# Performance work log

Hardware: AMD Instinct MI355X
Metric: run time of the kernel (lower is better)

Reference implementation:

```python
import jax, jax.numpy as jnp
import numpy as np

N_NODES = 100000
N_EDGES = 1000000
D = 64
HID = 64
OUT = 64
N_CLS = 10
N_GRAPHS = 512
BN_EPS = 1e-5


def setup_inputs() -> dict:
    key = jax.random.key(0)
    ks = jax.random.split(key, 16)
    inp = {
        "x": jax.random.normal(ks[0], (N_NODES, D), dtype=jnp.float32),
        "edge_index": jax.random.randint(ks[1], (2, N_EDGES), 0, N_NODES, dtype=jnp.int32),
        "batch": jnp.sort(jax.random.randint(ks[2], (N_NODES,), 0, N_GRAPHS, dtype=jnp.int32)),
    }
    def lin(k, fi, fo):
        lim = 1.0 / np.sqrt(fi)
        kw, kb = jax.random.split(k)
        return (jax.random.uniform(kw, (fi, fo), minval=-lim, maxval=lim, dtype=jnp.float32),
                jax.random.uniform(kb, (fo,), minval=-lim, maxval=lim, dtype=jnp.float32))
    # conv0 MLP([64,64,64]) with BN after first linear
    inp["w0a"], inp["b0a"] = lin(ks[3], D, HID)
    inp["g0"] = jnp.ones((HID,), jnp.float32); inp["be0"] = jnp.zeros((HID,), jnp.float32)
    inp["m0"] = jnp.zeros((HID,), jnp.float32); inp["v0"] = jnp.ones((HID,), jnp.float32)
    inp["w0b"], inp["b0b"] = lin(ks[4], HID, HID)
    # conv1 MLP([64,64,64])
    inp["w1a"], inp["b1a"] = lin(ks[5], HID, HID)
    inp["g1"] = jnp.ones((HID,), jnp.float32); inp["be1"] = jnp.zeros((HID,), jnp.float32)
    inp["m1"] = jnp.zeros((HID,), jnp.float32); inp["v1"] = jnp.ones((HID,), jnp.float32)
    inp["w1b"], inp["b1b"] = lin(ks[6], HID, OUT)
    # classifier
    inp["wc"], inp["bc"] = lin(ks[7], OUT, N_CLS)
    return inp


def _bn_eval(h, g, b, m, v):
    return (h - m) * jax.lax.rsqrt(v + BN_EPS) * g + b


def _mlp(h, wa, ba, g, be, m, v, wb, bb):
    # Linear -> BN -> ReLU -> (dropout eval=identity) -> Linear
    h = h @ wa + ba
    h = jax.nn.relu(_bn_eval(h, g, be, m, v))
    return h @ wb + bb


def _gin_conv(h, src, dst, wa, ba, g, be, m, v, wb, bb):
    # GINConv eps=0: mlp(x + sum_{j->i} x_j), messages scatter-added at dst
    agg = jax.ops.segment_sum(h[src], dst, num_segments=N_NODES)
    return _mlp(h + agg, wa, ba, g, be, m, v, wb, bb)


def reference(x, edge_index, batch,
              w0a, b0a, g0, be0, m0, v0, w0b, b0b,
              w1a, b1a, g1, be1, m1, v1, w1b, b1b,
              wc, bc):
    src, dst = edge_index[0], edge_index[1]
    h = _gin_conv(x, src, dst, w0a, b0a, g0, be0, m0, v0, w0b, b0b)
    h = jax.nn.relu(h)  # dropout is identity in eval
    h = _gin_conv(h, src, dst, w1a, b1a, g1, be1, m1, v1, w1b, b1b)
    # global mean pool over batch indices
    sums = jax.ops.segment_sum(h, batch, num_segments=N_GRAPHS)
    cnts = jax.ops.segment_sum(jnp.ones((h.shape[0],), h.dtype), batch, num_segments=N_GRAPHS)
    pooled = sums / jnp.maximum(cnts, 1.0)[:, None]
    return pooled @ wc + bc
```

## Files before the change

### kernel.cpp

```cpp
#include <hip/hip_runtime.h>

#define N_NODES 100000
#define N_EDGES 1000000
#define N_GRAPHS 512
#define N_CLS 10
#define BN_EPS 1e-5f

#define SCAN_NB 200
#define NTILES2 3125

typedef _Float16 half8 __attribute__((ext_vector_type(8)));
typedef _Float16 half4v __attribute__((ext_vector_type(4)));
typedef float floatx4 __attribute__((ext_vector_type(4)));

__global__ __launch_bounds__(256) void prep_kernel(
    const float* __restrict__ x, _Float16* __restrict__ xh,
    const int* __restrict__ batch, const int* __restrict__ dstI,
    int* __restrict__ deg, int* __restrict__ rank,
    const float* __restrict__ w0a, const float* __restrict__ b0a,
    const float* __restrict__ g0, const float* __restrict__ be0,
    const float* __restrict__ m0, const float* __restrict__ v0,
    const float* __restrict__ w0b,
    const float* __restrict__ w1a, const float* __restrict__ b1a,
    const float* __restrict__ g1, const float* __restrict__ be1,
    const float* __restrict__ m1, const float* __restrict__ v1,
    const float* __restrict__ w1b,
    int* __restrict__ gstart,
    _Float16* __restrict__ wHi, _Float16* __restrict__ wLo,
    float* __restrict__ b1p0, float* __restrict__ b1p1) {
    const int gid = blockIdx.x * 256 + threadIdx.x;

    if (gid < 1600000) {
        float4 v = ((const float4*)x)[gid];
        half4v h = {(_Float16)v.x, (_Float16)v.y, (_Float16)v.z, (_Float16)v.w};
        ((half4v*)xh)[gid] = h;
    }

    if (gid < N_EDGES)
        rank[gid] = atomicAdd(&deg[dstI[gid]], 1);

    if (gid <= N_NODES) {
        int bcur = (gid < N_NODES) ? batch[gid] : N_GRAPHS;
        int bprev = (gid > 0) ? batch[gid - 1] : -1;
        for (int g = bprev + 1; g <= bcur; ++g) gstart[g] = gid;
    }

    if (gid < 16384) {
        const int e = gid & 4095, mat = gid >> 12;
        const int jj = e & 7, lane = (e >> 3) & 63, c = (e >> 9) & 3, k0 = (e >> 11) & 1;
        const int k = k0 * 32 + (lane >> 4) * 8 + jj;
        const int col = c * 16 + (lane & 15);
        float val;
        if (mat == 0)      val = w0a[k * 64 + col] * (rsqrtf(v0[col] + BN_EPS) * g0[col]);
        else if (mat == 1) val = w0b[k * 64 + col];
        else if (mat == 2) val = w1a[k * 64 + col] * (rsqrtf(v1[col] + BN_EPS) * g1[col]);
        else               val = w1b[k * 64 + col];
        _Float16 hi = (_Float16)val;
        wHi[gid] = hi;
        wLo[gid] = (_Float16)(val - (float)hi);
    }

    if (gid >= 16384 && gid < 16512) {
        int t = gid - 16384;
        if (t < 64) {
            float s = rsqrtf(v0[t] + BN_EPS) * g0[t];
            b1p0[t] = (b0a[t] - m0[t]) * s + be0[t];
        } else {
            t -= 64;
            float s = rsqrtf(v1[t] + BN_EPS) * g1[t];
            b1p1[t] = (b1a[t] - m1[t]) * s + be1[t];
        }
    }
}

__global__ __launch_bounds__(256) void scanA_kernel(const int* __restrict__ deg,
                                                    int* __restrict__ bsum) {
    __shared__ int sh[256];
    const int base = blockIdx.x * 512;
    const int t = threadIdx.x;
    int a = 0, b = 0;
    if (base + t < N_NODES) a = deg[base + t];
    if (base + 256 + t < N_NODES) b = deg[base + 256 + t];
    sh[t] = a + b;
    __syncthreads();
#pragma unroll
    for (int off = 128; off > 0; off >>= 1) {
        if (t < off) sh[t] += sh[t + off];
        __syncthreads();
    }
    if (t == 0) bsum[blockIdx.x] = sh[0];
}

__global__ __launch_bounds__(256) void scanC_kernel(const int* __restrict__ deg,
                                                    const int* __restrict__ bsum,
                                                    int* __restrict__ rowptr) {
    __shared__ int sh[256];
    __shared__ int sboff[256];
    const int base = blockIdx.x * 512;
    const int t = threadIdx.x;

    const int bv = (t < SCAN_NB) ? bsum[t] : 0;
    sboff[t] = bv;

    const int i0 = base + 2 * t, i1 = i0 + 1;
    const int d0 = (i0 < N_NODES) ? deg[i0] : 0;
    const int d1 = (i1 < N_NODES) ? deg[i1] : 0;
    const int p = d0 + d1;
    sh[t] = p;
    __syncthreads();
#pragma unroll
    for (int off = 1; off < 256; off <<= 1) {
        int u = (t >= off) ? sh[t - off] : 0;
        int ub = (t >= off) ? sboff[t - off] : 0;
        __syncthreads();
        sh[t] += u;
        sboff[t] += ub;
        __syncthreads();
    }
    const int myoff = (blockIdx.x == 0) ? 0 : sboff[blockIdx.x - 1];
    const int excl = myoff + sh[t] - p;
    if (i0 < N_NODES) rowptr[i0] = excl;
    if (i1 < N_NODES) rowptr[i1] = excl + d0;
    if (blockIdx.x == 0 && t == 0) rowptr[N_NODES] = N_EDGES;
}

__global__ __launch_bounds__(256) void fill_kernel(const int* __restrict__ srcI,
                                                   const int* __restrict__ dstI,
                                                   const int* __restrict__ rank,
                                                   const int* __restrict__ rowptr,
                                                   int* __restrict__ sortedSrc) {
    int e = blockIdx.x * 256 + threadIdx.x;
    if (e >= N_EDGES) return;
    sortedSrc[rowptr[dstI[e]] + rank[e]] = srcI[e];
}

__device__ __forceinline__ int swz(int row, int col) {
    return row * 64 + (col ^ ((row & 7) << 3));
}

__device__ __forceinline__ void idx_stage(const int* __restrict__ srcList, int rpv,
                                          int mq, int nodeSel, int slotSel, int& idxOwn) {
    const int rr0 = __shfl(rpv, mq * 4 + nodeSel, 64);
    const int rr1 = __shfl(rpv, mq * 4 + nodeSel + 1, 64);
    const int c = rr1 - rr0;
    const int e0 = (c > 0) ? min(slotSel, c - 1) : 0;
    int pos = rr0 + e0;
    pos = min(pos, N_EDGES - 1);
    idxOwn = srcList[pos];
}

__device__ __forceinline__ void rows_stage(const _Float16* __restrict__ in, int rpv,
                                           int mq, int strip0, int eoff, int lf,
                                           int idxOwn, half4v (&vT)[4][4], half4v (&sS)[4]) {
    const int m0 = mq * 4;
#pragma unroll
    for (int i = 0; i < 4; ++i) {
        sS[i] = (half4v){0, 0, 0, 0};
        if (eoff == 0)
            sS[i] = *(const half4v*)(in + (size_t)(strip0 + m0 + i) * 64 + lf * 4);
    }
#pragma unroll
    for (int i = 0; i < 4; ++i) {
        const int rr0 = __builtin_amdgcn_readlane(rpv, m0 + i);
        const int rr1 = __builtin_amdgcn_readlane(rpv, m0 + i + 1);
        const int cI = rr1 - rr0;
        const int g = (min(cI, 16) + 3) >> 2;
#pragma unroll
        for (int k = 0; k < 4; ++k) {
            vT[i][k] = (half4v){0, 0, 0, 0};
            if (k < g) {
                const int id = __shfl(idxOwn, i * 16 + 4 * k + eoff, 64);
                vT[i][k] = *(const half4v*)(in + (size_t)id * 64 + lf * 4);
            }
        }
    }
}

__device__ __forceinline__ void consume_stage(const _Float16* __restrict__ in,
                                              const int* __restrict__ srcList, int rpv,
                                              int mq, int eoff, int lf, int j,
                                              const half4v (&vT)[4][4], const half4v (&sS)[4],
                                              _Float16* aggH, _Float16* aggL) {
    const int m0 = mq * 4;
#pragma unroll
    for (int i = 0; i < 4; ++i) {
        const int rr0 = __builtin_amdgcn_readlane(rpv, m0 + i);
        const int rr1 = __builtin_amdgcn_readlane(rpv, m0 + i + 1);
        const int cI = rr1 - rr0;
        float aR[4] = {0.f, 0.f, 0.f, 0.f};
#pragma unroll
        for (int k = 0; k < 4; ++k) {
            if (4 * k + eoff < cI) {
                aR[0] += (float)vT[i][k].x; aR[1] += (float)vT[i][k].y;
                aR[2] += (float)vT[i][k].z; aR[3] += (float)vT[i][k].w;
            }
        }
        for (int eb = 16; eb < cI; eb += 16) {
#pragma unroll
            for (int k = 0; k < 4; ++k) {
                const int e_ = eb + 4 * k + eoff;
                if (e_ < cI) {
                    const int id = srcList[rr0 + e_];
                    half4v t = *(const half4v*)(in + (size_t)id * 64 + lf * 4);
                    aR[0] += (float)t.x; aR[1] += (float)t.y;
                    aR[2] += (float)t.z; aR[3] += (float)t.w;
                }
            }
        }
        if (eoff == 0) {
            aR[0] += (float)sS[i].x; aR[1] += (float)sS[i].y;
            aR[2] += (float)sS[i].z; aR[3] += (float)sS[i].w;
        }
#pragma unroll
        for (int q = 0; q < 4; ++q) {
            aR[q] += __shfl_xor(aR[q], 16, 64);
            aR[q] += __shfl_xor(aR[q], 32, 64);
        }
        if (j < 16) {
            half4v hi, lo;
#pragma unroll
            for (int q = 0; q < 4; ++q) {
                hi[q] = (_Float16)aR[q];
                lo[q] = (_Float16)(aR[q] - (float)hi[q]);
            }
            const int idx = swz(m0 + i, 4 * j);
            *(half4v*)(aggH + idx) = hi;
            *(half4v*)(aggL + idx) = lo;
        }
    }
}

#define SBAR() __builtin_amdgcn_sched_barrier(0)

template <int POOL>
__global__ __launch_bounds__(128, 2) void conv_mfma(
    const _Float16* __restrict__ in, const int* __restrict__ rowptr,
    const int* __restrict__ srcList,
    const _Float16* __restrict__ wH1, const _Float16* __restrict__ wL1,
    const _Float16* __restrict__ wH2, const _Float16* __restrict__ wL2,
    const float* __restrict__ b1, const float* __restrict__ b2,
    _Float16* __restrict__ out, const int* __restrict__ batch,
    float* __restrict__ pooled) {
    __shared__ __align__(16) unsigned char scratch[2][4096];

    const int tid = threadIdx.x;
    const int j = tid & 63, wv = tid >> 6;
    const int eoff = j >> 4;
    const int lf = j & 15;
    const int base = blockIdx.x * 32;
    const int strip0 = base + wv * 16;

    int bb = 0;
    if (POOL) bb = batch[strip0 + min(j, 15)];

    const int rpv = rowptr[strip0 + min(j, 16)];

    _Float16* aggH = (_Float16*)scratch[wv];
    _Float16* aggL = aggH + 1024;

    {
        int idxA, idxB, idxC;
        half4v vA[4][4], vB[4][4], sA[4], sB[4];

        idx_stage(srcList, rpv, 0, eoff, lf, idxA);
        idx_stage(srcList, rpv, 1, eoff, lf, idxB);
        SBAR();
        rows_stage(in, rpv, 0, strip0, eoff, lf, idxA, vA, sA);
        SBAR();
        idx_stage(srcList, rpv, 2, eoff, lf, idxC);
        SBAR();
        rows_stage(in, rpv, 1, strip0, eoff, lf, idxB, vB, sB);
        SBAR();
        consume_stage(in, srcList, rpv, 0, eoff, lf, j, vA, sA, aggH, aggL);
        SBAR();
        idx_stage(srcList, rpv, 3, eoff, lf, idxA);
        SBAR();
        rows_stage(in, rpv, 2, strip0, eoff, lf, idxC, vA, sA);
        SBAR();
        consume_stage(in, srcList, rpv, 1, eoff, lf, j, vB, sB, aggH, aggL);
        SBAR();
        rows_stage(in, rpv, 3, strip0, eoff, lf, idxA, vB, sB);
        SBAR();
        consume_stage(in, srcList, rpv, 2, eoff, lf, j, vA, sA, aggH, aggL);
        SBAR();
        consume_stage(in, srcList, rpv, 3, eoff, lf, j, vB, sB, aggH, aggL);
    }

    const int l15 = j & 15, quad = j >> 4;
    const floatx4 vzero = {0.f, 0.f, 0.f, 0.f};

    floatx4 acc[4] = {vzero, vzero, vzero, vzero};
    {
#pragma unroll
        for (int k0 = 0; k0 < 2; ++k0) {
            const int aidx = swz(l15, quad * 8 + k0 * 32);
            half8 aH = *(const half8*)(aggH + aidx);
            half8 aL = *(const half8*)(aggL + aidx);
#pragma unroll
            for (int c = 0; c < 4; ++c) {
                const int fo = ((k0 * 4 + c) * 64 + j) * 8;
                half8 bH = *(const half8*)(wH1 + fo);
                half8 bL = *(const half8*)(wL1 + fo);
                acc[c] = __builtin_amdgcn_mfma_f32_16x16x32_f16(aH, bH, acc[c], 0, 0, 0);
                acc[c] = __builtin_amdgcn_mfma_f32_16x16x32_f16(aL, bH, acc[c], 0, 0, 0);
                acc[c] = __builtin_amdgcn_mfma_f32_16x16x32_f16(aH, bL, acc[c], 0, 0, 0);
            }
        }
    }
    _Float16* hH = aggH;
    _Float16* hL = aggL;
#pragma unroll
    for (int c = 0; c < 4; ++c) {
        const float bv = b1[c * 16 + l15];
#pragma unroll
        for (int r = 0; r < 4; ++r) {
            const int idx = swz(quad * 4 + r, c * 16 + l15);
            float v = acc[c][r] + bv;
            v = fmaxf(v, 0.f);
            const _Float16 hi = (_Float16)v;
            hH[idx] = hi;
            hL[idx] = (_Float16)(v - (float)hi);
        }
    }

    floatx4 acc2[4] = {vzero, vzero, vzero, vzero};
    {
#pragma unroll
        for (int k0 = 0; k0 < 2; ++k0) {
            const int aidx = swz(l15, quad * 8 + k0 * 32);
            half8 aH = *(const half8*)(hH + aidx);
            half8 aL = *(const half8*)(hL + aidx);
#pragma unroll
            for (int c = 0; c < 4; ++c) {
                const int fo = ((k0 * 4 + c) * 64 + j) * 8;
                half8 bH = *(const half8*)(wH2 + fo);
                half8 bL = *(const half8*)(wL2 + fo);
                acc2[c] = __builtin_amdgcn_mfma_f32_16x16x32_f16(aH, bH, acc2[c], 0, 0, 0);
                acc2[c] = __builtin_amdgcn_mfma_f32_16x16x32_f16(aL, bH, acc2[c], 0, 0, 0);
                acc2[c] = __builtin_amdgcn_mfma_f32_16x16x32_f16(aH, bL, acc2[c], 0, 0, 0);
            }
        }
    }

    if (!POOL) {
#pragma unroll
        for (int c = 0; c < 4; ++c) {
            const float bv = b2[c * 16 + l15];
#pragma unroll
            for (int r = 0; r < 4; ++r) {
                const int node = strip0 + quad * 4 + r;
                out[(size_t)node * 64 + c * 16 + l15] =
                    (_Float16)fmaxf(acc2[c][r] + bv, 0.f);
            }
        }
    } else {
        float* oT = (float*)scratch[wv];
#pragma unroll
        for (int c = 0; c < 4; ++c) {
            const float bv = b2[c * 16 + l15];
#pragma unroll
            for (int r = 0; r < 4; ++r)
                oT[(quad * 4 + r) * 64 + c * 16 + l15] = acc2[c][r] + bv;
        }
        __builtin_amdgcn_s_waitcnt(0);
        int curB = -1;
        float accv = 0.f;
#pragma unroll
        for (int r = 0; r < 16; ++r) {
            const int b = __builtin_amdgcn_readlane(bb, r);
            const float v = oT[r * 64 + j];
            if (b != curB) {
                if (curB >= 0) atomicAdd(&pooled[curB * 64 + j], accv);
                curB = b;
                accv = v;
            } else {
                accv += v;
            }
        }
        atomicAdd(&pooled[curB * 64 + j], accv);
    }
}

__global__ __launch_bounds__(64) void classifier_kernel(const float* __restrict__ pooled,
                                                        const int* __restrict__ gstart,
                                                        const float* __restrict__ wc,
                                                        const float* __restrict__ bc,
                                                        float* __restrict__ out) {
    const int g = blockIdx.x;
    const int j = threadIdx.x;
    const float c = fmaxf((float)(gstart[g + 1] - gstart[g]), 1.f);
    const float mean = pooled[g * 64 + j] / c;
#pragma unroll
    for (int cc = 0; cc < N_CLS; ++cc) {
        float p = mean * wc[j * N_CLS + cc];
#pragma unroll
        for (int off = 32; off > 0; off >>= 1) p += __shfl_down(p, off, 64);
        if (j == 0) out[g * N_CLS + cc] = p + bc[cc];
    }
}


extern "C" void kernel_launch(void* const* d_in, const int* in_sizes, int n_in,
                              void* d_out, int out_size, void* d_ws, size_t ws_size,
                              hipStream_t stream) {
    const float* x   = (const float*)d_in[0];
    const int*   ei  = (const int*)d_in[1];
    const int* batch = (const int*)d_in[2];
    const float* w0a = (const float*)d_in[3];
    const float* b0a = (const float*)d_in[4];
    const float* g0  = (const float*)d_in[5];
    const float* be0 = (const float*)d_in[6];
    const float* m0  = (const float*)d_in[7];
    const float* v0  = (const float*)d_in[8];
    const float* w0b = (const float*)d_in[9];
    const float* b0b = (const float*)d_in[10];
    const float* w1a = (const float*)d_in[11];
    const float* b1a = (const float*)d_in[12];
    const float* g1  = (const float*)d_in[13];
    const float* be1 = (const float*)d_in[14];
    const float* m1  = (const float*)d_in[15];
    const float* v1  = (const float*)d_in[16];
    const float* w1b = (const float*)d_in[17];
    const float* b1b = (const float*)d_in[18];
    const float* wc  = (const float*)d_in[19];
    const float* bc  = (const float*)d_in[20];
    float* out = (float*)d_out;

    const int* srcI = ei;
    const int* dstI = ei + N_EDGES;

    int* ws = (int*)d_ws;
    int*      deg       = ws;
    int*      bsum      = ws + 100000;
    float*    pooled    = (float*)(ws + 100404);
    int*      rowptr    = ws + 133172;
    int*      rank      = ws + 233176;
    int*      sortedSrc = ws + 1233176;
    _Float16* xh        = (_Float16*)(ws + 2233176);
    _Float16* h1        = (_Float16*)(ws + 5433176);
    float*    b1p0      = (float*)(ws + 8633176);
    float*    b1p1      = (float*)(ws + 8633240);
    int*      gstart    = ws + 8633304;
    _Float16* wHi       = (_Float16*)(ws + 8633820);
    _Float16* wLo       = (_Float16*)(ws + 8642012);

    (void)hipMemsetAsync((void*)deg, 0, 133172 * sizeof(int), stream);
    prep_kernel<<<6250, 256, 0, stream>>>(x, xh, batch, dstI, deg, rank,
                                          w0a, b0a, g0, be0, m0, v0, w0b,
                                          w1a, b1a, g1, be1, m1, v1, w1b,
                                          gstart, wHi, wLo, b1p0, b1p1);

    scanA_kernel<<<SCAN_NB, 256, 0, stream>>>(deg, bsum);
    scanC_kernel<<<SCAN_NB, 256, 0, stream>>>(deg, bsum, rowptr);
    fill_kernel<<<(N_EDGES + 255) / 256, 256, 0, stream>>>(srcI, dstI, rank, rowptr, sortedSrc);

    conv_mfma<0><<<NTILES2, 128, 0, stream>>>(xh, rowptr, sortedSrc,
                                              wHi, wLo, wHi + 4096, wLo + 4096,
                                              b1p0, b0b, h1, nullptr, nullptr);

    conv_mfma<1><<<NTILES2, 128, 0, stream>>>(h1, rowptr, sortedSrc,
                                              wHi + 8192, wLo + 8192, wHi + 12288, wLo + 12288,
                                              b1p1, b1b, nullptr, batch, pooled);

    classifier_kernel<<<N_GRAPHS, 64, 0, stream>>>(pooled, gstart, wc, bc, out);
}
```

Before: 279.4 us.

## Replace per-edge rank array with atomic cursor fill and move fp16 conversion

The degree count no longer records a per-edge rank. The CSR fill now takes slots through an atomic cursor initialised by the scan, which removes the 4 MB rank write and read. The x-to-fp16 conversion moves from the prep kernel into the fill kernel, so prep launches fewer blocks and the conversion shares a launch with the fill. In exchange the fill kernel issues atomics on a second pass, and the order of sources within each row becomes nondeterministic.

```diff
diff --git a/kernel.cpp b/kernel.cpp
--- a/kernel.cpp
+++ b/kernel.cpp
@@ -14,9 +14,8 @@
 typedef float floatx4 __attribute__((ext_vector_type(4)));
 
 __global__ __launch_bounds__(256) void prep_kernel(
-    const float* __restrict__ x, _Float16* __restrict__ xh,
     const int* __restrict__ batch, const int* __restrict__ dstI,
-    int* __restrict__ deg, int* __restrict__ rank,
+    int* __restrict__ deg,
     const float* __restrict__ w0a, const float* __restrict__ b0a,
     const float* __restrict__ g0, const float* __restrict__ be0,
     const float* __restrict__ m0, const float* __restrict__ v0,
@@ -30,14 +29,8 @@
     float* __restrict__ b1p0, float* __restrict__ b1p1) {
     const int gid = blockIdx.x * 256 + threadIdx.x;
 
-    if (gid < 1600000) {
-        float4 v = ((const float4*)x)[gid];
-        half4v h = {(_Float16)v.x, (_Float16)v.y, (_Float16)v.z, (_Float16)v.w};
-        ((half4v*)xh)[gid] = h;
-    }
-
     if (gid < N_EDGES)
-        rank[gid] = atomicAdd(&deg[dstI[gid]], 1);
+        atomicAdd(&deg[dstI[gid]], 1);
 
     if (gid <= N_NODES) {
         int bcur = (gid < N_NODES) ? batch[gid] : N_GRAPHS;
@@ -93,7 +86,8 @@
 
 __global__ __launch_bounds__(256) void scanC_kernel(const int* __restrict__ deg,
                                                     const int* __restrict__ bsum,
-                                                    int* __restrict__ rowptr) {
+                                                    int* __restrict__ rowptr,
+                                                    int* __restrict__ cursor) {
     __shared__ int sh[256];
     __shared__ int sboff[256];
     const int base = blockIdx.x * 512;
@@ -119,19 +113,29 @@
     }
     const int myoff = (blockIdx.x == 0) ? 0 : sboff[blockIdx.x - 1];
     const int excl = myoff + sh[t] - p;
-    if (i0 < N_NODES) rowptr[i0] = excl;
-    if (i1 < N_NODES) rowptr[i1] = excl + d0;
+    if (i0 < N_NODES) { rowptr[i0] = excl;      cursor[i0] = excl; }
+    if (i1 < N_NODES) { rowptr[i1] = excl + d0; cursor[i1] = excl + d0; }
     if (blockIdx.x == 0 && t == 0) rowptr[N_NODES] = N_EDGES;
 }
 
-__global__ __launch_bounds__(256) void fill_kernel(const int* __restrict__ srcI,
+__global__ __launch_bounds__(256) void fill_kernel(const float* __restrict__ x,
+                                                   _Float16* __restrict__ xh,
+                                                   const int* __restrict__ srcI,
                                                    const int* __restrict__ dstI,
-                                                   const int* __restrict__ rank,
-                                                   const int* __restrict__ rowptr,
+                                                   int* __restrict__ cursor,
                                                    int* __restrict__ sortedSrc) {
-    int e = blockIdx.x * 256 + threadIdx.x;
-    if (e >= N_EDGES) return;
-    sortedSrc[rowptr[dstI[e]] + rank[e]] = srcI[e];
+    const int gid = blockIdx.x * 256 + threadIdx.x;
+
+    if (gid < 1600000) {
+        float4 v = ((const float4*)x)[gid];
+        half4v h = {(_Float16)v.x, (_Float16)v.y, (_Float16)v.z, (_Float16)v.w};
+        ((half4v*)xh)[gid] = h;
+    }
+
+    if (gid < N_EDGES) {
+        const int pos = atomicAdd(&cursor[dstI[gid]], 1);
+        sortedSrc[pos] = srcI[gid];
+    }
 }
 
 __device__ __forceinline__ int swz(int row, int col) {
@@ -434,7 +438,7 @@
     int*      bsum      = ws + 100000;
     float*    pooled    = (float*)(ws + 100404);
     int*      rowptr    = ws + 133172;
-    int*      rank      = ws + 233176;
+    int*      cursor    = ws + 233176;
     int*      sortedSrc = ws + 1233176;
     _Float16* xh        = (_Float16*)(ws + 2233176);
     _Float16* h1        = (_Float16*)(ws + 5433176);
@@ -445,14 +449,16 @@
     _Float16* wLo       = (_Float16*)(ws + 8642012);
 
     (void)hipMemsetAsync((void*)deg, 0, 133172 * sizeof(int), stream);
-    prep_kernel<<<6250, 256, 0, stream>>>(x, xh, batch, dstI, deg, rank,
+
+    prep_kernel<<<3907, 256, 0, stream>>>(batch, dstI, deg,
                                           w0a, b0a, g0, be0, m0, v0, w0b,
                                           w1a, b1a, g1, be1, m1, v1, w1b,
                                           gstart, wHi, wLo, b1p0, b1p1);
 
     scanA_kernel<<<SCAN_NB, 256, 0, stream>>>(deg, bsum);
-    scanC_kernel<<<SCAN_NB, 256, 0, stream>>>(deg, bsum, rowptr);
-    fill_kernel<<<(N_EDGES + 255) / 256, 256, 0, stream>>>(srcI, dstI, rank, rowptr, sortedSrc);
+    scanC_kernel<<<SCAN_NB, 256, 0, stream>>>(deg, bsum, rowptr, cursor);
+
+    fill_kernel<<<6250, 256, 0, stream>>>(x, xh, srcI, dstI, cursor, sortedSrc);
 
     conv_mfma<0><<<NTILES2, 128, 0, stream>>>(xh, rowptr, sortedSrc,
                                               wHi, wLo, wHi + 4096, wLo + 4096,
```

Result: slower. 320.9 us (+14.9%).
